# Performance work log

Measured on AMD Instinct MI355X. Metric: run time of the kernel, lower is better.

Reference implementation:

```python
import jax, jax.numpy as jnp
import numpy as np

B, N, DEG = 128, 512, 8          # graphs, nodes per graph, avg degree
E = B * N * DEG                  # 524288 edges
F_IN, H1, H2, C = 128, 64, 128, 10
RATIO = 0.8
K = int(np.ceil(RATIO * N))      # TopKPooling keeps ceil(0.8*N)=410 nodes per graph


def setup_inputs() -> dict:
    key = jax.random.key(0)
    ks = jax.random.split(key, 10)
    n_nodes = B * N
    x = jax.random.normal(ks[0], (n_nodes, F_IN), dtype=jnp.float32)
    # random intra-graph edges, then offset node ids per graph
    src = jax.random.randint(ks[1], (B, N * DEG), 0, N)
    dst = jax.random.randint(ks[2], (B, N * DEG), 0, N)
    off = (jnp.arange(B) * N)[:, None]
    edge_index = jnp.stack([(src + off).reshape(-1), (dst + off).reshape(-1)]).astype(jnp.int64)
    batch = jnp.repeat(jnp.arange(B), N).astype(jnp.int64)
    s1 = 1.0 / np.sqrt(F_IN)
    s2 = 1.0 / np.sqrt(H1)
    s3 = 1.0 / np.sqrt(H2)
    return {
        "x": x,
        "edge_index": edge_index,
        "batch": batch,
        "W1": jax.random.uniform(ks[3], (F_IN, H1), jnp.float32, -s1, s1),
        "b1": jnp.zeros((H1,), jnp.float32),
        "W2": jax.random.uniform(ks[4], (H1, H2), jnp.float32, -s2, s2),
        "b2": jnp.zeros((H2,), jnp.float32),
        "pool_w": jax.random.uniform(ks[5], (H2,), jnp.float32, -s3, s3),
        "fc_W": jax.random.uniform(ks[6], (H2, C), jnp.float32, -s3, s3),
        "fc_b": jax.random.uniform(ks[7], (C,), jnp.float32, -s3, s3),
    }


def gcn_conv(x, W, b, src, dst, num_nodes):
    # PyG GCNConv: add self-loops, symmetric normalization, scatter-add aggregation
    loop = jnp.arange(num_nodes)
    src = jnp.concatenate([src, loop])
    dst = jnp.concatenate([dst, loop])
    deg = jax.ops.segment_sum(jnp.ones_like(src, dtype=x.dtype), dst, num_segments=num_nodes)
    dis = jnp.where(deg > 0, jax.lax.rsqrt(jnp.maximum(deg, 1.0)), 0.0)
    norm = dis[src] * dis[dst]                       # [E+N]
    h = x @ W                                        # transform first (smaller of the two in conv1)
    out = jax.ops.segment_sum(norm[:, None] * h[src], dst, num_segments=num_nodes)
    return out + b


def reference(x, edge_index, batch, W1, b1, W2, b2, pool_w, fc_W, fc_b):
    num_nodes = x.shape[0]
    src, dst = edge_index[0], edge_index[1]
    x = jax.nn.relu(gcn_conv(x, W1, b1, src, dst, num_nodes))
    x = jax.nn.relu(gcn_conv(x, W2, b2, src, dst, num_nodes))
    # TopKPooling: score = (x . w)/||w||, per-graph top-k on raw score, gate by tanh(score)
    score = (x @ pool_w) / jnp.linalg.norm(pool_w)   # [B*N]
    score_b = score.reshape(B, N)
    top_vals, top_idx = jax.lax.top_k(score_b, K)    # [B, K]
    x_b = x.reshape(B, N, H2)
    x_sel = jnp.take_along_axis(x_b, top_idx[:, :, None], axis=1)   # [B, K, H2]
    x_sel = x_sel * jnp.tanh(top_vals)[:, :, None]
    # global max pool over each (pooled) graph; pooled edge_index is unused downstream
    g = jnp.max(x_sel, axis=1)                        # [B, H2]
    logits = g @ fc_W + fc_b                          # [B, C]
    return jax.nn.log_softmax(logits, axis=1)
```

## Files before the change

kernel.cpp:

```cpp
#include <hip/hip_runtime.h>
#include <hip/hip_bf16.h>


#define BB 128
#define NN 512
#define NODES (BB*NN)
#define EE (BB*NN*8)
#define EDGPG (NN*8)
#define F_IN 128
#define H1 64
#define H2 128
#define NC 10
#define KSEL 410
#define EPG (NN*8 + NN)
#define TOT_ADJ (EE + NODES)

typedef unsigned short u16;
typedef unsigned int   u32;

static __device__ __forceinline__ float lo2f(u32 u){ return __uint_as_float(u << 16); }
static __device__ __forceinline__ float hi2f(u32 u){ return __uint_as_float(u & 0xffff0000u); }
static __device__ __forceinline__ u16 f2b(float f){
    __hip_bfloat16 h = __float2bfloat16(f);
    return *reinterpret_cast<u16*>(&h);
}
static __device__ __forceinline__ u32 packbf(float a, float b){
    return (u32)f2b(a) | ((u32)f2b(b) << 16);
}

static __device__ __forceinline__ bool ei_is_i64(const int* __restrict__ ei){
    return ((ei[1] | ei[3] | ei[5] | ei[7]) == 0);
}
static __device__ __forceinline__ int ld_src(const int* __restrict__ ei, int e, bool w64){
    return w64 ? ei[2*e] : ei[e];
}
static __device__ __forceinline__ int ld_dst(const int* __restrict__ ei, int e, bool w64){
    return w64 ? ei[2*(EE + e)] : ei[EE + e];
}

__global__ __launch_bounds__(512) void k_build(const int* __restrict__ ei,
                                               int* __restrict__ row_start,
                                               int* __restrict__ cnt_g,
                                               float* __restrict__ dis,
                                               int* __restrict__ adj){
    __shared__ int cnt[NN];
    __shared__ int sh[NN];
    __shared__ int cur[NN];
    bool w64 = ei_is_i64(ei);
    int b = blockIdx.x, t = threadIdx.x;
    cnt[t] = 0;
    __syncthreads();
    int e0 = b*EDGPG;
    for (int i = t; i < EDGPG; i += 512){
        int d = (ld_dst(ei, e0 + i, w64) - b*NN) & (NN - 1);
        atomicAdd(&cnt[d], 1);
    }
    __syncthreads();
    int tot = cnt[t] + 1;
    sh[t] = tot;
    __syncthreads();
    for (int off = 1; off < NN; off <<= 1){
        int v = (t >= off) ? sh[t-off] : 0;
        __syncthreads();
        sh[t] += v;
        __syncthreads();
    }
    int rs_local = sh[t] - tot;
    row_start[b*NN + t] = b*EPG + rs_local;
    cnt_g[b*NN + t]     = tot - 1;
    dis[b*NN + t]       = rsqrtf((float)tot);
    cur[t] = rs_local;
    __syncthreads();
    {
        int p = atomicAdd(&cur[t], 1);
        adj[b*EPG + p] = b*NN + t;
    }
    for (int i = t; i < EDGPG; i += 512){
        int d = (ld_dst(ei, e0 + i, w64) - b*NN) & (NN - 1);
        int s = ld_src(ei, e0 + i, w64) & (NODES - 1);
        int p = atomicAdd(&cur[d], 1);
        adj[b*EPG + p] = s;
    }
}

#define G1NODES 64
#define XPAD 68
__global__ __launch_bounds__(256) void k_gemm1(const float* __restrict__ x,
                                               const float* __restrict__ W1,
                                               const float* __restrict__ dis,
                                               u32* __restrict__ h1u){
    __shared__ __align__(16) float Ws[64*H1];
    __shared__ __align__(16) float xs[G1NODES*XPAD];
    int t = threadIdx.x;
    int node0 = blockIdx.x*G1NODES;
    int tc = t & 15, tr = t >> 4;
    int j0 = tc*4, n0 = tr*4;
    float acc[4][4] = {};
    for (int half = 0; half < 2; ++half){
        const float4* Wv = (const float4*)(W1 + half*4096);
        for (int i = t; i < 1024; i += 256)
            *(float4*)&Ws[i*4] = Wv[i];
        for (int i = t; i < 1024; i += 256){
            int node = i >> 4, c = i & 15;
            float4 v = *(const float4*)(x + (size_t)(node0 + node)*F_IN + half*64 + c*4);
            *(float4*)&xs[node*XPAD + c*4] = v;
        }
        __syncthreads();
        #pragma unroll 4
        for (int k = 0; k < 64; ++k){
            float4 wv = *(const float4*)&Ws[k*H1 + j0];
            float x0 = xs[(n0+0)*XPAD + k];
            float x1 = xs[(n0+1)*XPAD + k];
            float x2 = xs[(n0+2)*XPAD + k];
            float x3 = xs[(n0+3)*XPAD + k];
            acc[0][0] += x0*wv.x; acc[0][1] += x0*wv.y; acc[0][2] += x0*wv.z; acc[0][3] += x0*wv.w;
            acc[1][0] += x1*wv.x; acc[1][1] += x1*wv.y; acc[1][2] += x1*wv.z; acc[1][3] += x1*wv.w;
            acc[2][0] += x2*wv.x; acc[2][1] += x2*wv.y; acc[2][2] += x2*wv.z; acc[2][3] += x2*wv.w;
            acc[3][0] += x3*wv.x; acc[3][1] += x3*wv.y; acc[3][2] += x3*wv.z; acc[3][3] += x3*wv.w;
        }
        __syncthreads();
    }
    #pragma unroll
    for (int i = 0; i < 4; ++i){
        float dn = dis[node0 + n0 + i];
        size_t base = (size_t)(node0 + n0 + i)*32 + tc*2;
        h1u[base]     = packbf(dn*acc[i][0], dn*acc[i][1]);
        h1u[base + 1] = packbf(dn*acc[i][2], dn*acc[i][3]);
    }
}

__global__ __launch_bounds__(256) void k_agg1(const uint2* __restrict__ h1v,
                                              const int* __restrict__ row_start,
                                              const int* __restrict__ cnt,
                                              const int* __restrict__ adj,
                                              const float* __restrict__ dis,
                                              const float4* __restrict__ b1v,
                                              uint2* __restrict__ a1v){
    int t = threadIdx.x;
    int node = blockIdx.x*16 + (t >> 4);
    int fl = t & 15;
    int rs = row_start[node];
    int deg = cnt[node] + 1; if (deg > EPG) deg = EPG;
    int pe = rs + deg;
    float a0[4] = {}, a1r[4] = {}, a2r[4] = {}, a3r[4] = {};
    int p = rs;
    for (; p + 4 <= pe; p += 4){
        int s0 = adj[p], s1 = adj[p+1], s2 = adj[p+2], s3 = adj[p+3];
        uint2 v0 = h1v[s0*16 + fl];
        uint2 v1 = h1v[s1*16 + fl];
        uint2 v2 = h1v[s2*16 + fl];
        uint2 v3 = h1v[s3*16 + fl];
        a0[0] += lo2f(v0.x); a0[1] += hi2f(v0.x); a0[2] += lo2f(v0.y); a0[3] += hi2f(v0.y);
        a1r[0] += lo2f(v1.x); a1r[1] += hi2f(v1.x); a1r[2] += lo2f(v1.y); a1r[3] += hi2f(v1.y);
        a2r[0] += lo2f(v2.x); a2r[1] += hi2f(v2.x); a2r[2] += lo2f(v2.y); a2r[3] += hi2f(v2.y);
        a3r[0] += lo2f(v3.x); a3r[1] += hi2f(v3.x); a3r[2] += lo2f(v3.y); a3r[3] += hi2f(v3.y);
    }
    for (; p < pe; ++p){
        int s = adj[p];
        uint2 v = h1v[s*16 + fl];
        a0[0] += lo2f(v.x); a0[1] += hi2f(v.x); a0[2] += lo2f(v.y); a0[3] += hi2f(v.y);
    }
    float r0 = (a0[0] + a1r[0]) + (a2r[0] + a3r[0]);
    float r1 = (a0[1] + a1r[1]) + (a2r[1] + a3r[1]);
    float r2 = (a0[2] + a1r[2]) + (a2r[2] + a3r[2]);
    float r3 = (a0[3] + a1r[3]) + (a2r[3] + a3r[3]);
    float dn = dis[node];
    float4 bb = b1v[fl];
    float w0 = dn*r0 + bb.x; w0 = w0 > 0.f ? w0 : 0.f;
    float w1 = dn*r1 + bb.y; w1 = w1 > 0.f ? w1 : 0.f;
    float w2 = dn*r2 + bb.z; w2 = w2 > 0.f ? w2 : 0.f;
    float w3 = dn*r3 + bb.w; w3 = w3 > 0.f ? w3 : 0.f;
    a1v[node*16 + fl] = make_uint2(packbf(dn*w0, dn*w1), packbf(dn*w2, dn*w3));
}

#define G2NODES 32
#define APAD 68
__global__ __launch_bounds__(256) void k_gemm2s(const uint2* __restrict__ a1v,
                                                const int* __restrict__ row_start,
                                                const int* __restrict__ cnt,
                                                const int* __restrict__ adj,
                                                const float* __restrict__ dis,
                                                const float* __restrict__ W2,
                                                const float* __restrict__ b2,
                                                const float* __restrict__ pw,
                                                u32* __restrict__ a2u,
                                                float* __restrict__ score){
    __shared__ __align__(16) float Ws[32*H2];
    __shared__ __align__(16) float as[G2NODES*APAD];
    __shared__ float pws[H2];
    int t = threadIdx.x;
    int node0 = blockIdx.x*G2NODES;
    if (t < H2) pws[t] = pw[t];
    {
        int fl = t & 15, ng = t >> 4;
        for (int pass = 0; pass < 2; ++pass){
            int nl = ng + pass*16;
            int node = node0 + nl;
            int rs = row_start[node];
            int deg = cnt[node] + 1; if (deg > EPG) deg = EPG;
            int pe = rs + deg;
            float a0[4] = {}, a1r[4] = {}, a2r[4] = {}, a3r[4] = {};
            int p = rs;
            for (; p + 4 <= pe; p += 4){
                int s0 = adj[p], s1 = adj[p+1], s2 = adj[p+2], s3 = adj[p+3];
                uint2 v0 = a1v[s0*16 + fl];
                uint2 v1 = a1v[s1*16 + fl];
                uint2 v2 = a1v[s2*16 + fl];
                uint2 v3 = a1v[s3*16 + fl];
                a0[0] += lo2f(v0.x); a0[1] += hi2f(v0.x); a0[2] += lo2f(v0.y); a0[3] += hi2f(v0.y);
                a1r[0] += lo2f(v1.x); a1r[1] += hi2f(v1.x); a1r[2] += lo2f(v1.y); a1r[3] += hi2f(v1.y);
                a2r[0] += lo2f(v2.x); a2r[1] += hi2f(v2.x); a2r[2] += lo2f(v2.y); a2r[3] += hi2f(v2.y);
                a3r[0] += lo2f(v3.x); a3r[1] += hi2f(v3.x); a3r[2] += lo2f(v3.y); a3r[3] += hi2f(v3.y);
            }
            for (; p < pe; ++p){
                int s = adj[p];
                uint2 v = a1v[s*16 + fl];
                a0[0] += lo2f(v.x); a0[1] += hi2f(v.x); a0[2] += lo2f(v.y); a0[3] += hi2f(v.y);
            }
            float dn = dis[node];
            float* dst = &as[nl*APAD + 4*fl];
            dst[0] = dn*((a0[0] + a1r[0]) + (a2r[0] + a3r[0]));
            dst[1] = dn*((a0[1] + a1r[1]) + (a2r[1] + a3r[1]));
            dst[2] = dn*((a0[2] + a1r[2]) + (a2r[2] + a3r[2]));
            dst[3] = dn*((a0[3] + a1r[3]) + (a2r[3] + a3r[3]));
        }
    }
    int tc = t & 31, tr = t >> 5;
    int j0 = tc*4, n0 = tr*4;
    float acc[4][4] = {};
    for (int half = 0; half < 2; ++half){
        const float4* Wv = (const float4*)(W2 + half*4096);
        for (int i = t; i < 1024; i += 256)
            *(float4*)&Ws[i*4] = Wv[i];
        __syncthreads();
        int kb = half*32;
        #pragma unroll 4
        for (int k = 0; k < 32; ++k){
            float4 wv = *(const float4*)&Ws[k*H2 + j0];
            float x0 = as[(n0+0)*APAD + kb + k];
            float x1 = as[(n0+1)*APAD + kb + k];
            float x2 = as[(n0+2)*APAD + kb + k];
            float x3 = as[(n0+3)*APAD + kb + k];
            acc[0][0] += x0*wv.x; acc[0][1] += x0*wv.y; acc[0][2] += x0*wv.z; acc[0][3] += x0*wv.w;
            acc[1][0] += x1*wv.x; acc[1][1] += x1*wv.y; acc[1][2] += x1*wv.z; acc[1][3] += x1*wv.w;
            acc[2][0] += x2*wv.x; acc[2][1] += x2*wv.y; acc[2][2] += x2*wv.z; acc[2][3] += x2*wv.w;
            acc[3][0] += x3*wv.x; acc[3][1] += x3*wv.y; acc[3][2] += x3*wv.z; acc[3][3] += x3*wv.w;
        }
        __syncthreads();
    }
    float p0 = pws[j0], p1 = pws[j0+1], p2 = pws[j0+2], p3 = pws[j0+3];
    float bj0 = b2[j0], bj1 = b2[j0+1], bj2 = b2[j0+2], bj3 = b2[j0+3];
    #pragma unroll
    for (int i = 0; i < 4; ++i){
        float v0 = acc[i][0] + bj0; v0 = v0 > 0.f ? v0 : 0.f;
        float v1 = acc[i][1] + bj1; v1 = v1 > 0.f ? v1 : 0.f;
        float v2 = acc[i][2] + bj2; v2 = v2 > 0.f ? v2 : 0.f;
        float v3 = acc[i][3] + bj3; v3 = v3 > 0.f ? v3 : 0.f;
        size_t base = (size_t)(node0 + n0 + i)*64 + tc*2;
        a2u[base]     = packbf(v0, v1);
        a2u[base + 1] = packbf(v2, v3);
        float sp = v0*p0 + v1*p1 + v2*p2 + v3*p3;
        sp += __shfl_xor(sp, 16, 32);
        sp += __shfl_xor(sp,  8, 32);
        sp += __shfl_xor(sp,  4, 32);
        sp += __shfl_xor(sp,  2, 32);
        sp += __shfl_xor(sp,  1, 32);
        if (tc == 0) score[node0 + n0 + i] = sp;
    }
}

__global__ __launch_bounds__(512) void k_pool(const u32* __restrict__ a2u,
                                              const float* __restrict__ score,
                                              const float* __restrict__ pw,
                                              const float* __restrict__ fcW,
                                              const float* __restrict__ fcb,
                                              float* __restrict__ out){
    __shared__ float so[NN];
    __shared__ float ss[NN];
    __shared__ float th[NN];
    __shared__ float pm[16*H2];
    __shared__ float gl[H2];
    __shared__ float fws[H2*NC];
    __shared__ float lg[NC];
    __shared__ float red[3];
    int b = blockIdx.x, t = threadIdx.x;
    for (int i = t; i < H2*NC; i += 512) fws[i] = fcW[i];
    if (t < H2){ float v = pw[t]; gl[t] = v*v; }
    __syncthreads();
    if (t == 0){
        float s = 0.f;
        for (int i = 0; i < H2; ++i) s += gl[i];
        red[2] = rsqrtf(s);
    }
    __syncthreads();
    float pwinv = red[2];
    float sc = score[b*NN + t];
    so[t] = sc; ss[t] = sc; th[t] = tanhf(sc*pwinv);
    __syncthreads();
    for (int k = 2; k <= NN; k <<= 1){
        for (int j = k >> 1; j > 0; j >>= 1){
            int ixj = t ^ j;
            if (ixj > t){
                float a = ss[t], c = ss[ixj];
                bool desc = ((t & k) == 0);
                bool sw = desc ? (a < c) : (a > c);
                if (sw){ ss[t] = c; ss[ixj] = a; }
            }
            __syncthreads();
        }
    }
    float thresh = ss[KSEL-1];
    float mask_t = (so[t] >= thresh) ? 0.f : -INFINITY;
    __syncthreads();
    so[t] = mask_t;
    __syncthreads();
    int tc = t & 31, q = t >> 5;
    const uint2* ap = (const uint2*)(a2u + (size_t)b*NN*64);
    float m0 = -INFINITY, m1 = -INFINITY, m2 = -INFINITY, m3 = -INFINITY;
    int nb = q*32;
    #pragma unroll 4
    for (int n = nb; n < nb + 32; ++n){
        uint2 v = ap[(size_t)n*32 + tc];
        float thn = th[n], son = so[n];
        m0 = fmaxf(m0, lo2f(v.x)*thn + son);
        m1 = fmaxf(m1, hi2f(v.x)*thn + son);
        m2 = fmaxf(m2, lo2f(v.y)*thn + son);
        m3 = fmaxf(m3, hi2f(v.y)*thn + son);
    }
    pm[q*H2 + 4*tc]     = m0;
    pm[q*H2 + 4*tc + 1] = m1;
    pm[q*H2 + 4*tc + 2] = m2;
    pm[q*H2 + 4*tc + 3] = m3;
    __syncthreads();
    if (t < H2){
        float g = pm[t];
        #pragma unroll
        for (int qq = 1; qq < 16; ++qq) g = fmaxf(g, pm[qq*H2 + t]);
        gl[t] = g;
    }
    __syncthreads();
    if (t < NC){
        float acc = fcb[t];
        for (int k2 = 0; k2 < H2; ++k2) acc += gl[k2]*fws[k2*NC + t];
        lg[t] = acc;
    }
    __syncthreads();
    if (t == 0){
        float mx = lg[0];
        for (int i = 1; i < NC; ++i) mx = fmaxf(mx, lg[i]);
        float s = 0.f;
        for (int i = 0; i < NC; ++i) s += expf(lg[i] - mx);
        red[0] = mx; red[1] = logf(s);
    }
    __syncthreads();
    if (t < NC) out[b*NC + t] = lg[t] - red[0] - red[1];
}

extern "C" void kernel_launch(void* const* d_in, const int* in_sizes, int n_in,
                              void* d_out, int out_size, void* d_ws, size_t ws_size,
                              hipStream_t stream) {
    const float* x   = (const float*)d_in[0];
    const int*   ei  = (const int*)d_in[1];
    const float* W1  = (const float*)d_in[3];
    const float* b1  = (const float*)d_in[4];
    const float* W2  = (const float*)d_in[5];
    const float* b2  = (const float*)d_in[6];
    const float* pw  = (const float*)d_in[7];
    const float* fcW = (const float*)d_in[8];
    const float* fcb = (const float*)d_in[9];

    char* ws = (char*)d_ws;
    int*   cnt       = (int*)(ws + 4096);
    int*   row_start = (int*)(ws + 266240);
    float* dis       = (float*)(ws + 528384);
    float* score     = (float*)(ws + 790528);
    int*   adj       = (int*)(ws + 1052672);
    u32*   h1u       = (u32*)(ws + 4194304);
    u32*   a1u       = (u32*)(ws + 12582912);
    u32*   a2u       = (u32*)(ws + 20971520);

    k_build<<<BB, 512, 0, stream>>>(ei, row_start, cnt, dis, adj);
    k_gemm1<<<NODES/G1NODES, 256, 0, stream>>>(x, W1, dis, h1u);
    k_agg1<<<NODES/16, 256, 0, stream>>>((const uint2*)h1u, row_start, cnt, adj, dis,
                                         (const float4*)b1, (uint2*)a1u);
    k_gemm2s<<<NODES/G2NODES, 256, 0, stream>>>((const uint2*)a1u, row_start, cnt, adj,
                                                dis, W2, b2, pw, a2u, score);
    k_pool<<<BB, 512, 0, stream>>>(a2u, score, pw, fcW, fcb, (float*)d_out);
}
```

Measured before the change: 179.3 us.

## Widen gathers to 16-byte loads, cache edge dsts in LDS, vectorize GEMM LDS reads

The aggregation kernels now gather 8 bf16 features per thread with uint4 loads, so 8 lanes cover a node instead of 16 and each block handles twice as many nodes. The pooling max reduction uses the same wider loads. k_build keeps the destination indices in shared memory so the second pass does not re-read them from global memory. Both GEMM inner loops read x/activation values as float4 from LDS. Together these cut instruction count and memory transactions per gathered row, but double accumulator registers in the gather loops, which may reduce occupancy.

```diff
diff --git a/kernel.cpp b/kernel.cpp
--- a/kernel.cpp
+++ b/kernel.cpp
@@ -27,6 +27,12 @@
 static __device__ __forceinline__ u32 packbf(float a, float b){
     return (u32)f2b(a) | ((u32)f2b(b) << 16);
 }
+static __device__ __forceinline__ void acc8(float* a, uint4 v){
+    a[0] += lo2f(v.x); a[1] += hi2f(v.x);
+    a[2] += lo2f(v.y); a[3] += hi2f(v.y);
+    a[4] += lo2f(v.z); a[5] += hi2f(v.z);
+    a[6] += lo2f(v.w); a[7] += hi2f(v.w);
+}
 
 static __device__ __forceinline__ bool ei_is_i64(const int* __restrict__ ei){
     return ((ei[1] | ei[3] | ei[5] | ei[7]) == 0);
@@ -46,6 +52,7 @@
     __shared__ int cnt[NN];
     __shared__ int sh[NN];
     __shared__ int cur[NN];
+    __shared__ u16 ldst[EDGPG];
     bool w64 = ei_is_i64(ei);
     int b = blockIdx.x, t = threadIdx.x;
     cnt[t] = 0;
@@ -53,6 +60,7 @@
     int e0 = b*EDGPG;
     for (int i = t; i < EDGPG; i += 512){
         int d = (ld_dst(ei, e0 + i, w64) - b*NN) & (NN - 1);
+        ldst[i] = (u16)d;
         atomicAdd(&cnt[d], 1);
     }
     __syncthreads();
@@ -76,7 +84,7 @@
         adj[b*EPG + p] = b*NN + t;
     }
     for (int i = t; i < EDGPG; i += 512){
-        int d = (ld_dst(ei, e0 + i, w64) - b*NN) & (NN - 1);
+        int d = (int)ldst[i];
         int s = ld_src(ei, e0 + i, w64) & (NODES - 1);
         int p = atomicAdd(&cur[d], 1);
         adj[b*EPG + p] = s;
@@ -106,17 +114,24 @@
             *(float4*)&xs[node*XPAD + c*4] = v;
         }
         __syncthreads();
-        #pragma unroll 4
-        for (int k = 0; k < 64; ++k){
-            float4 wv = *(const float4*)&Ws[k*H1 + j0];
-            float x0 = xs[(n0+0)*XPAD + k];
-            float x1 = xs[(n0+1)*XPAD + k];
-            float x2 = xs[(n0+2)*XPAD + k];
-            float x3 = xs[(n0+3)*XPAD + k];
-            acc[0][0] += x0*wv.x; acc[0][1] += x0*wv.y; acc[0][2] += x0*wv.z; acc[0][3] += x0*wv.w;
-            acc[1][0] += x1*wv.x; acc[1][1] += x1*wv.y; acc[1][2] += x1*wv.z; acc[1][3] += x1*wv.w;
-            acc[2][0] += x2*wv.x; acc[2][1] += x2*wv.y; acc[2][2] += x2*wv.z; acc[2][3] += x2*wv.w;
-            acc[3][0] += x3*wv.x; acc[3][1] += x3*wv.y; acc[3][2] += x3*wv.z; acc[3][3] += x3*wv.w;
+        #pragma unroll 2
+        for (int k = 0; k < 64; k += 4){
+            float4 xv0 = *(const float4*)&xs[(n0+0)*XPAD + k];
+            float4 xv1 = *(const float4*)&xs[(n0+1)*XPAD + k];
+            float4 xv2 = *(const float4*)&xs[(n0+2)*XPAD + k];
+            float4 xv3 = *(const float4*)&xs[(n0+3)*XPAD + k];
+            float xa0[4] = {xv0.x, xv0.y, xv0.z, xv0.w};
+            float xa1[4] = {xv1.x, xv1.y, xv1.z, xv1.w};
+            float xa2[4] = {xv2.x, xv2.y, xv2.z, xv2.w};
+            float xa3[4] = {xv3.x, xv3.y, xv3.z, xv3.w};
+            #pragma unroll
+            for (int kk = 0; kk < 4; ++kk){
+                float4 wv = *(const float4*)&Ws[(k+kk)*H1 + j0];
+                acc[0][0] += xa0[kk]*wv.x; acc[0][1] += xa0[kk]*wv.y; acc[0][2] += xa0[kk]*wv.z; acc[0][3] += xa0[kk]*wv.w;
+                acc[1][0] += xa1[kk]*wv.x; acc[1][1] += xa1[kk]*wv.y; acc[1][2] += xa1[kk]*wv.z; acc[1][3] += xa1[kk]*wv.w;
+                acc[2][0] += xa2[kk]*wv.x; acc[2][1] += xa2[kk]*wv.y; acc[2][2] += xa2[kk]*wv.z; acc[2][3] += xa2[kk]*wv.w;
+                acc[3][0] += xa3[kk]*wv.x; acc[3][1] += xa3[kk]*wv.y; acc[3][2] += xa3[kk]*wv.z; acc[3][3] += xa3[kk]*wv.w;
+            }
         }
         __syncthreads();
     }
@@ -129,53 +144,53 @@
     }
 }
 
-__global__ __launch_bounds__(256) void k_agg1(const uint2* __restrict__ h1v,
+__global__ __launch_bounds__(256) void k_agg1(const uint4* __restrict__ h1v,
                                               const int* __restrict__ row_start,
                                               const int* __restrict__ cnt,
                                               const int* __restrict__ adj,
                                               const float* __restrict__ dis,
                                               const float4* __restrict__ b1v,
-                                              uint2* __restrict__ a1v){
+                                              uint4* __restrict__ a1v){
     int t = threadIdx.x;
-    int node = blockIdx.x*16 + (t >> 4);
-    int fl = t & 15;
+    int node = blockIdx.x*32 + (t >> 3);
+    int fl = t & 7;
     int rs = row_start[node];
     int deg = cnt[node] + 1; if (deg > EPG) deg = EPG;
     int pe = rs + deg;
-    float a0[4] = {}, a1r[4] = {}, a2r[4] = {}, a3r[4] = {};
+    float a0[8] = {}, a1r[8] = {}, a2r[8] = {}, a3r[8] = {};
     int p = rs;
     for (; p + 4 <= pe; p += 4){
         int s0 = adj[p], s1 = adj[p+1], s2 = adj[p+2], s3 = adj[p+3];
-        uint2 v0 = h1v[s0*16 + fl];
-        uint2 v1 = h1v[s1*16 + fl];
-        uint2 v2 = h1v[s2*16 + fl];
-        uint2 v3 = h1v[s3*16 + fl];
-        a0[0] += lo2f(v0.x); a0[1] += hi2f(v0.x); a0[2] += lo2f(v0.y); a0[3] += hi2f(v0.y);
-        a1r[0] += lo2f(v1.x); a1r[1] += hi2f(v1.x); a1r[2] += lo2f(v1.y); a1r[3] += hi2f(v1.y);
-        a2r[0] += lo2f(v2.x); a2r[1] += hi2f(v2.x); a2r[2] += lo2f(v2.y); a2r[3] += hi2f(v2.y);
-        a3r[0] += lo2f(v3.x); a3r[1] += hi2f(v3.x); a3r[2] += lo2f(v3.y); a3r[3] += hi2f(v3.y);
+        uint4 v0 = h1v[s0*8 + fl];
+        uint4 v1 = h1v[s1*8 + fl];
+        uint4 v2 = h1v[s2*8 + fl];
+        uint4 v3 = h1v[s3*8 + fl];
+        acc8(a0, v0); acc8(a1r, v1); acc8(a2r, v2); acc8(a3r, v3);
     }
     for (; p < pe; ++p){
-        int s = adj[p];
-        uint2 v = h1v[s*16 + fl];
-        a0[0] += lo2f(v.x); a0[1] += hi2f(v.x); a0[2] += lo2f(v.y); a0[3] += hi2f(v.y);
-    }
-    float r0 = (a0[0] + a1r[0]) + (a2r[0] + a3r[0]);
-    float r1 = (a0[1] + a1r[1]) + (a2r[1] + a3r[1]);
-    float r2 = (a0[2] + a1r[2]) + (a2r[2] + a3r[2]);
-    float r3 = (a0[3] + a1r[3]) + (a2r[3] + a3r[3]);
+        uint4 v = h1v[adj[p]*8 + fl];
+        acc8(a0, v);
+    }
+    float r[8];
+    #pragma unroll
+    for (int j = 0; j < 8; ++j) r[j] = (a0[j] + a1r[j]) + (a2r[j] + a3r[j]);
     float dn = dis[node];
-    float4 bb = b1v[fl];
-    float w0 = dn*r0 + bb.x; w0 = w0 > 0.f ? w0 : 0.f;
-    float w1 = dn*r1 + bb.y; w1 = w1 > 0.f ? w1 : 0.f;
-    float w2 = dn*r2 + bb.z; w2 = w2 > 0.f ? w2 : 0.f;
-    float w3 = dn*r3 + bb.w; w3 = w3 > 0.f ? w3 : 0.f;
-    a1v[node*16 + fl] = make_uint2(packbf(dn*w0, dn*w1), packbf(dn*w2, dn*w3));
+    float4 bA = b1v[2*fl], bB = b1v[2*fl+1];
+    float w0 = dn*r[0] + bA.x; w0 = w0 > 0.f ? w0 : 0.f;
+    float w1 = dn*r[1] + bA.y; w1 = w1 > 0.f ? w1 : 0.f;
+    float w2 = dn*r[2] + bA.z; w2 = w2 > 0.f ? w2 : 0.f;
+    float w3 = dn*r[3] + bA.w; w3 = w3 > 0.f ? w3 : 0.f;
+    float w4 = dn*r[4] + bB.x; w4 = w4 > 0.f ? w4 : 0.f;
+    float w5 = dn*r[5] + bB.y; w5 = w5 > 0.f ? w5 : 0.f;
+    float w6 = dn*r[6] + bB.z; w6 = w6 > 0.f ? w6 : 0.f;
+    float w7 = dn*r[7] + bB.w; w7 = w7 > 0.f ? w7 : 0.f;
+    a1v[node*8 + fl] = make_uint4(packbf(dn*w0, dn*w1), packbf(dn*w2, dn*w3),
+                                  packbf(dn*w4, dn*w5), packbf(dn*w6, dn*w7));
 }
 
 #define G2NODES 32
 #define APAD 68
-__global__ __launch_bounds__(256) void k_gemm2s(const uint2* __restrict__ a1v,
+__global__ __launch_bounds__(256) void k_gemm2s(const uint4* __restrict__ a1v,
                                                 const int* __restrict__ row_start,
                                                 const int* __restrict__ cnt,
                                                 const int* __restrict__ adj,
@@ -192,38 +207,37 @@
     int node0 = blockIdx.x*G2NODES;
     if (t < H2) pws[t] = pw[t];
     {
-        int fl = t & 15, ng = t >> 4;
-        for (int pass = 0; pass < 2; ++pass){
-            int nl = ng + pass*16;
-            int node = node0 + nl;
-            int rs = row_start[node];
-            int deg = cnt[node] + 1; if (deg > EPG) deg = EPG;
-            int pe = rs + deg;
-            float a0[4] = {}, a1r[4] = {}, a2r[4] = {}, a3r[4] = {};
-            int p = rs;
-            for (; p + 4 <= pe; p += 4){
-                int s0 = adj[p], s1 = adj[p+1], s2 = adj[p+2], s3 = adj[p+3];
-                uint2 v0 = a1v[s0*16 + fl];
-                uint2 v1 = a1v[s1*16 + fl];
-                uint2 v2 = a1v[s2*16 + fl];
-                uint2 v3 = a1v[s3*16 + fl];
-                a0[0] += lo2f(v0.x); a0[1] += hi2f(v0.x); a0[2] += lo2f(v0.y); a0[3] += hi2f(v0.y);
-                a1r[0] += lo2f(v1.x); a1r[1] += hi2f(v1.x); a1r[2] += lo2f(v1.y); a1r[3] += hi2f(v1.y);
-                a2r[0] += lo2f(v2.x); a2r[1] += hi2f(v2.x); a2r[2] += lo2f(v2.y); a2r[3] += hi2f(v2.y);
-                a3r[0] += lo2f(v3.x); a3r[1] += hi2f(v3.x); a3r[2] += lo2f(v3.y); a3r[3] += hi2f(v3.y);
-            }
-            for (; p < pe; ++p){
-                int s = adj[p];
-                uint2 v = a1v[s*16 + fl];
-                a0[0] += lo2f(v.x); a0[1] += hi2f(v.x); a0[2] += lo2f(v.y); a0[3] += hi2f(v.y);
-            }
-            float dn = dis[node];
-            float* dst = &as[nl*APAD + 4*fl];
-            dst[0] = dn*((a0[0] + a1r[0]) + (a2r[0] + a3r[0]));
-            dst[1] = dn*((a0[1] + a1r[1]) + (a2r[1] + a3r[1]));
-            dst[2] = dn*((a0[2] + a1r[2]) + (a2r[2] + a3r[2]));
-            dst[3] = dn*((a0[3] + a1r[3]) + (a2r[3] + a3r[3]));
-        }
+        int fl = t & 7, nl = t >> 3;
+        int node = node0 + nl;
+        int rs = row_start[node];
+        int deg = cnt[node] + 1; if (deg > EPG) deg = EPG;
+        int pe = rs + deg;
+        float a0[8] = {}, a1r[8] = {}, a2r[8] = {}, a3r[8] = {};
+        int p = rs;
+        for (; p + 4 <= pe; p += 4){
+            int s0 = adj[p], s1 = adj[p+1], s2 = adj[p+2], s3 = adj[p+3];
+            uint4 v0 = a1v[s0*8 + fl];
+            uint4 v1 = a1v[s1*8 + fl];
+            uint4 v2 = a1v[s2*8 + fl];
+            uint4 v3 = a1v[s3*8 + fl];
+            acc8(a0, v0); acc8(a1r, v1); acc8(a2r, v2); acc8(a3r, v3);
+        }
+        for (; p < pe; ++p){
+            uint4 v = a1v[adj[p]*8 + fl];
+            acc8(a0, v);
+        }
+        float dn = dis[node];
+        float* dst = &as[nl*APAD + 8*fl];
+        float r0 = dn*((a0[0] + a1r[0]) + (a2r[0] + a3r[0]));
+        float r1 = dn*((a0[1] + a1r[1]) + (a2r[1] + a3r[1]));
+        float r2 = dn*((a0[2] + a1r[2]) + (a2r[2] + a3r[2]));
+        float r3 = dn*((a0[3] + a1r[3]) + (a2r[3] + a3r[3]));
+        float r4 = dn*((a0[4] + a1r[4]) + (a2r[4] + a3r[4]));
+        float r5 = dn*((a0[5] + a1r[5]) + (a2r[5] + a3r[5]));
+        float r6 = dn*((a0[6] + a1r[6]) + (a2r[6] + a3r[6]));
+        float r7 = dn*((a0[7] + a1r[7]) + (a2r[7] + a3r[7]));
+        *(float4*)&dst[0] = make_float4(r0, r1, r2, r3);
+        *(float4*)&dst[4] = make_float4(r4, r5, r6, r7);
     }
     int tc = t & 31, tr = t >> 5;
     int j0 = tc*4, n0 = tr*4;
@@ -234,17 +248,24 @@
             *(float4*)&Ws[i*4] = Wv[i];
         __syncthreads();
         int kb = half*32;
-        #pragma unroll 4
-        for (int k = 0; k < 32; ++k){
-            float4 wv = *(const float4*)&Ws[k*H2 + j0];
-            float x0 = as[(n0+0)*APAD + kb + k];
-            float x1 = as[(n0+1)*APAD + kb + k];
-            float x2 = as[(n0+2)*APAD + kb + k];
-            float x3 = as[(n0+3)*APAD + kb + k];
-            acc[0][0] += x0*wv.x; acc[0][1] += x0*wv.y; acc[0][2] += x0*wv.z; acc[0][3] += x0*wv.w;
-            acc[1][0] += x1*wv.x; acc[1][1] += x1*wv.y; acc[1][2] += x1*wv.z; acc[1][3] += x1*wv.w;
-            acc[2][0] += x2*wv.x; acc[2][1] += x2*wv.y; acc[2][2] += x2*wv.z; acc[2][3] += x2*wv.w;
-            acc[3][0] += x3*wv.x; acc[3][1] += x3*wv.y; acc[3][2] += x3*wv.z; acc[3][3] += x3*wv.w;
+        #pragma unroll 2
+        for (int k = 0; k < 32; k += 4){
+            float4 xv0 = *(const float4*)&as[(n0+0)*APAD + kb + k];
+            float4 xv1 = *(const float4*)&as[(n0+1)*APAD + kb + k];
+            float4 xv2 = *(const float4*)&as[(n0+2)*APAD + kb + k];
+            float4 xv3 = *(const float4*)&as[(n0+3)*APAD + kb + k];
+            float xa0[4] = {xv0.x, xv0.y, xv0.z, xv0.w};
+            float xa1[4] = {xv1.x, xv1.y, xv1.z, xv1.w};
+            float xa2[4] = {xv2.x, xv2.y, xv2.z, xv2.w};
+            float xa3[4] = {xv3.x, xv3.y, xv3.z, xv3.w};
+            #pragma unroll
+            for (int kk = 0; kk < 4; ++kk){
+                float4 wv = *(const float4*)&Ws[(k+kk)*H2 + j0];
+                acc[0][0] += xa0[kk]*wv.x; acc[0][1] += xa0[kk]*wv.y; acc[0][2] += xa0[kk]*wv.z; acc[0][3] += xa0[kk]*wv.w;
+                acc[1][0] += xa1[kk]*wv.x; acc[1][1] += xa1[kk]*wv.y; acc[1][2] += xa1[kk]*wv.z; acc[1][3] += xa1[kk]*wv.w;
+                acc[2][0] += xa2[kk]*wv.x; acc[2][1] += xa2[kk]*wv.y; acc[2][2] += xa2[kk]*wv.z; acc[2][3] += xa2[kk]*wv.w;
+                acc[3][0] += xa3[kk]*wv.x; acc[3][1] += xa3[kk]*wv.y; acc[3][2] += xa3[kk]*wv.z; acc[3][3] += xa3[kk]*wv.w;
+            }
         }
         __syncthreads();
     }
@@ -278,7 +299,7 @@
     __shared__ float so[NN];
     __shared__ float ss[NN];
     __shared__ float th[NN];
-    __shared__ float pm[16*H2];
+    __shared__ float pm[32*H2];
     __shared__ float gl[H2];
     __shared__ float fws[H2*NC];
     __shared__ float lg[NC];
@@ -314,28 +335,32 @@
     __syncthreads();
     so[t] = mask_t;
     __syncthreads();
-    int tc = t & 31, q = t >> 5;
-    const uint2* ap = (const uint2*)(a2u + (size_t)b*NN*64);
+    int tc = t & 15, q = t >> 4;
+    const uint4* ap = (const uint4*)(a2u + (size_t)b*NN*64);
     float m0 = -INFINITY, m1 = -INFINITY, m2 = -INFINITY, m3 = -INFINITY;
-    int nb = q*32;
+    float m4 = -INFINITY, m5 = -INFINITY, m6 = -INFINITY, m7 = -INFINITY;
+    int nb = q*16;
     #pragma unroll 4
-    for (int n = nb; n < nb + 32; ++n){
-        uint2 v = ap[(size_t)n*32 + tc];
+    for (int n = nb; n < nb + 16; ++n){
+        uint4 v = ap[(size_t)n*16 + tc];
         float thn = th[n], son = so[n];
         m0 = fmaxf(m0, lo2f(v.x)*thn + son);
         m1 = fmaxf(m1, hi2f(v.x)*thn + son);
         m2 = fmaxf(m2, lo2f(v.y)*thn + son);
         m3 = fmaxf(m3, hi2f(v.y)*thn + son);
-    }
-    pm[q*H2 + 4*tc]     = m0;
-    pm[q*H2 + 4*tc + 1] = m1;
-    pm[q*H2 + 4*tc + 2] = m2;
-    pm[q*H2 + 4*tc + 3] = m3;
+        m4 = fmaxf(m4, lo2f(v.z)*thn + son);
+        m5 = fmaxf(m5, hi2f(v.z)*thn + son);
+        m6 = fmaxf(m6, lo2f(v.w)*thn + son);
+        m7 = fmaxf(m7, hi2f(v.w)*thn + son);
+    }
+    float* pmr = &pm[q*H2 + 8*tc];
+    pmr[0] = m0; pmr[1] = m1; pmr[2] = m2; pmr[3] = m3;
+    pmr[4] = m4; pmr[5] = m5; pmr[6] = m6; pmr[7] = m7;
     __syncthreads();
     if (t < H2){
         float g = pm[t];
         #pragma unroll
-        for (int qq = 1; qq < 16; ++qq) g = fmaxf(g, pm[qq*H2 + t]);
+        for (int qq = 1; qq < 32; ++qq) g = fmaxf(g, pm[qq*H2 + t]);
         gl[t] = g;
     }
     __syncthreads();
@@ -381,9 +406,9 @@
 
     k_build<<<BB, 512, 0, stream>>>(ei, row_start, cnt, dis, adj);
     k_gemm1<<<NODES/G1NODES, 256, 0, stream>>>(x, W1, dis, h1u);
-    k_agg1<<<NODES/16, 256, 0, stream>>>((const uint2*)h1u, row_start, cnt, adj, dis,
-                                         (const float4*)b1, (uint2*)a1u);
-    k_gemm2s<<<NODES/G2NODES, 256, 0, stream>>>((const uint2*)a1u, row_start, cnt, adj,
+    k_agg1<<<NODES/32, 256, 0, stream>>>((const uint4*)h1u, row_start, cnt, adj, dis,
+                                         (const float4*)b1, (uint4*)a1u);
+    k_gemm2s<<<NODES/G2NODES, 256, 0, stream>>>((const uint4*)a1u, row_start, cnt, adj,
                                                 dis, W2, b2, pw, a2u, score);
     k_pool<<<BB, 512, 0, stream>>>(a2u, score, pw, fcW, fcb, (float*)d_out);
 }
```

Measured after the change: 176.3 us. About the same (-1.7%).
